# Kernel optimization log

Hardware: AMD Instinct MI355X
Metric: run time of the kernel (lower is better)

## Reference

```python
import jax, jax.numpy as jnp
import numpy as np

B, L, D = 128, 196, 512
T = 20
V, E, H, A = 10000, 256, 512, 512


def setup_inputs() -> dict:
    key = jax.random.key(0)
    ks = jax.random.split(key, 20)
    s = lambda *sh: 0.02
    inp = {
        "a": jax.random.normal(ks[0], (B, L, D), jnp.float32),
        "captions": jax.random.randint(ks[1], (B, T), 0, V),
        "lengths": jnp.full((B,), T, dtype=jnp.int64),
        "embed_W": jax.random.normal(ks[2], (V, E), jnp.float32) * 0.02,
        "Wa": jax.random.normal(ks[3], (D, A), jnp.float32) * 0.02,
        "Wh": jax.random.normal(ks[4], (H, A), jnp.float32) * 0.02,
        "Wc": jax.random.normal(ks[5], (H, A), jnp.float32) * 0.02,
        "v": jax.random.normal(ks[6], (A,), jnp.float32) * 0.02,
        "beta_W": jax.random.normal(ks[7], (H, 1), jnp.float32) * 0.02,
        "beta_b": jnp.zeros((1,), jnp.float32),
        "W_ih": jax.random.normal(ks[8], (E + D, 4 * H), jnp.float32) * 0.02,
        "W_hh": jax.random.normal(ks[9], (H, 4 * H), jnp.float32) * 0.02,
        "b_ih": jnp.zeros((4 * H,), jnp.float32),
        "b_hh": jnp.zeros((4 * H,), jnp.float32),
        "fc_W": jax.random.normal(ks[10], (H, V), jnp.float32) * 0.02,
        "fc_b": jnp.zeros((V,), jnp.float32),
        "initW_h": jax.random.normal(ks[11], (D, H), jnp.float32) * 0.02,
        "initb_h": jnp.zeros((H,), jnp.float32),
        "initW_c": jax.random.normal(ks[12], (D, H), jnp.float32) * 0.02,
        "initb_c": jnp.zeros((H,), jnp.float32),
    }
    return inp


def _decode(a, captions, embed_W, Wa, Wh, Wc, v, beta_W, beta_b,
            W_ih, W_hh, b_ih, b_hh, fc_W, fc_b,
            initW_h, initb_h, initW_c, initb_c):
    # dropout layers are treated as identity (eval mode) for a deterministic reference
    emb = embed_W[captions]                       # (B, T, E)
    mean_ctx = a.mean(axis=1)                     # (B, D)
    h0 = jnp.tanh(mean_ctx @ initW_h + initb_h)   # (B, H)
    c0 = jnp.tanh(mean_ctx @ initW_c + initb_c)
    wa = a @ Wa                                   # (B, L, A), hoisted (invariant over t)
    Hd = h0.shape[-1]

    def step(carry, x_t):
        h, c, prev_h = carry
        # dual additive attention: scores from annotations + h + prev_h (context_input)
        score = jnp.tanh(wa + (h @ Wh)[:, None, :] + (prev_h @ Wc)[:, None, :])  # (B,L,A)
        e = score @ v                                                            # (B,L)
        alpha = jax.nn.softmax(e, axis=1)
        beta = jax.nn.sigmoid(h @ beta_W + beta_b)                               # (B,1)
        ctx = beta * jnp.einsum('bl,bld->bd', alpha, a)                          # (B,D)
        # LSTMCell
        x = jnp.concatenate([x_t, ctx], axis=1)                                  # (B,E+D)
        gates = x @ W_ih + b_ih + h @ W_hh + b_hh                                # (B,4H)
        i, f, g, o = jnp.split(gates, 4, axis=1)
        c_new = jax.nn.sigmoid(f) * c + jax.nn.sigmoid(i) * jnp.tanh(g)
        h_new = jax.nn.sigmoid(o) * jnp.tanh(c_new)
        logits_t = h_new @ fc_W + fc_b                                           # (B,V)
        return (h_new, c_new, h_new), (logits_t, alpha)

    xs = jnp.swapaxes(emb[:, :T - 1, :], 0, 1)    # (T-1, B, E) time-major
    _, (logits_t, alphas_t) = jax.lax.scan(step, (h0, c0, h0), xs)
    # all lengths == T: pack_padded_sequence(batch_first=True).data is time-major flatten
    packed_logits = logits_t.reshape((T - 1) * a.shape[0], -1)                   # ((T-1)*B, V)
    alphas = jnp.swapaxes(alphas_t, 0, 1)                                        # (B, T-1, L)
    return packed_logits, alphas


def reference(a, captions, lengths, embed_W, Wa, Wh, Wc, v, beta_W, beta_b,
              W_ih, W_hh, b_ih, b_hh, fc_W, fc_b,
              initW_h, initb_h, initW_c, initb_c):
    return _decode(a, captions, embed_W, Wa, Wh, Wc, v, beta_W, beta_b,
                   W_ih, W_hh, b_ih, b_hh, fc_W, fc_b,
                   initW_h, initb_h, initW_c, initb_c)
```

## Files before the change

kernel.cpp:

```cpp
#include <hip/hip_runtime.h>
#include <hip/hip_bf16.h>
#include <math.h>

#define B_ 128
#define L_ 196
#define D_ 512
#define T_ 20
#define V_ 10000
#define E_ 256
#define H_ 512
#define A_ 512
#define TM1 19
#define ROWS (TM1*B_)
#define G4H 2048
#define KCAT 1024
#define LH 98

typedef unsigned short ushort_t;
typedef __attribute__((ext_vector_type(8))) short bf16x8;
typedef __attribute__((ext_vector_type(4))) float f32x4;

__device__ __forceinline__ float fast_tanh(float x){
    float ax = fabsf(x);
    float e = __expf(-2.f*ax);
    float r = __builtin_amdgcn_rcpf(1.f + e);
    return copysignf((1.f - e)*r, x);
}
__device__ __forceinline__ float sigmoidf_(float x){
    return __builtin_amdgcn_rcpf(1.f + __expf(-x));
}
__device__ __forceinline__ ushort_t f2b(float f){
    union{float f; unsigned u;} x; x.f = f;
    unsigned r = x.u + 0x7fffu + ((x.u>>16)&1u);
    return (ushort_t)(r>>16);
}
__device__ __forceinline__ float b2f(ushort_t h){
    union{unsigned u; float f;} x; x.u = ((unsigned)h)<<16;
    return x.f;
}
__device__ __forceinline__ float b2f_lo(unsigned u){ union{unsigned u; float f;} x; x.u = u<<16; return x.f; }
__device__ __forceinline__ float b2f_hi(unsigned u){ union{unsigned u; float f;} x; x.u = u & 0xffff0000u; return x.f; }

template<int OUT_BF16, int HAS_BIAS, int NT, int SWZ>
__global__ __launch_bounds__(256)
void gemm_mfma(const ushort_t* __restrict__ A, int lda,
               const ushort_t* __restrict__ BT, int ldb,
               void* __restrict__ Cout, int ldc,
               int N, int K, const float* __restrict__ bias)
{
    __shared__ ushort_t As[128*32];
    __shared__ ushort_t Bs[128*32];
    int bm, bn;
    if (SWZ){
        int bid = blockIdx.x;
        int swz = (bid & 7)*190 + (bid >> 3);
        int mt = swz % 19, nt = swz / 19;
        if (nt >= 79) return;
        bm = mt*128; bn = nt*128;
    } else {
        bm = blockIdx.y * 128; bn = blockIdx.x * 128;
    }
    const int tid = threadIdx.x;
    const int lane = tid & 63;
    const int wave = tid >> 6;
    const int wm = (wave >> 1) * 64;
    const int wn = (wave & 1) * 64;
    const int lrow = lane & 15;
    const int lk8  = (lane >> 4) * 8;
    const int srow = tid >> 2;
    const int skq  = ((tid & 3) * 8) ^ ((srow & 3) << 3);
    const int skq0 = (tid & 3) * 8;

    f32x4 acc[4][4];
    #pragma unroll
    for (int i=0;i<4;i++)
        #pragma unroll
        for (int j=0;j<4;j++) acc[i][j] = (f32x4){0.f,0.f,0.f,0.f};

    const ushort_t* Abase = A  + (size_t)(bm+srow)*lda + skq0;
    const ushort_t* Bbase = BT + (size_t)(bn+srow)*ldb + skq0;

    for (int k0 = 0; k0 < K; k0 += 32) {
        int4 a0 = *(const int4*)(Abase + k0);
        int4 a1 = *(const int4*)(Abase + (size_t)64*lda + k0);
        int4 b0 = *(const int4*)(Bbase + k0);
        int4 b1 = *(const int4*)(Bbase + (size_t)64*ldb + k0);
        __syncthreads();
        *(int4*)&As[srow*32 + skq]      = a0;
        *(int4*)&As[(srow+64)*32 + skq] = a1;
        *(int4*)&Bs[srow*32 + skq]      = b0;
        *(int4*)&Bs[(srow+64)*32 + skq] = b1;
        __syncthreads();
        bf16x8 af[4], bfr[4];
        #pragma unroll
        for (int i=0;i<4;i++){
            int r = wm + i*16 + lrow;
            af[i]  = *(bf16x8*)&As[r*32 + (lk8 ^ ((r & 3) << 3))];
        }
        #pragma unroll
        for (int j=0;j<4;j++){
            int r = wn + j*16 + lrow;
            bfr[j] = *(bf16x8*)&Bs[r*32 + (lk8 ^ ((r & 3) << 3))];
        }
        #pragma unroll
        for (int i=0;i<4;i++)
            #pragma unroll
            for (int j=0;j<4;j++)
                acc[i][j] = __builtin_amdgcn_mfma_f32_16x16x32_bf16(af[i], bfr[j], acc[i][j], 0, 0, 0);
    }

    const int rq = (lane >> 4) * 4;
    #pragma unroll
    for (int j=0;j<4;j++){
        int col = bn + wn + j*16 + lrow;
        if (col >= N) continue;
        float bv = HAS_BIAS ? bias[col] : 0.f;
        #pragma unroll
        for (int i=0;i<4;i++){
            #pragma unroll
            for (int q=0;q<4;q++){
                int row = bm + wm + i*16 + rq + q;
                float v = acc[i][j][q] + bv;
                if (OUT_BF16) ((ushort_t*)Cout)[(size_t)row*ldc + col] = f2b(v);
                else if (NT)  __builtin_nontemporal_store(v, &((float*)Cout)[(size_t)row*ldc + col]);
                else          ((float*)Cout)[(size_t)row*ldc + col] = v;
            }
        }
    }
}

__global__ __launch_bounds__(256) void gemm64t2(const float* __restrict__ A, int lda,
                       const float* __restrict__ B0, const float* __restrict__ B1, int ldb,
                       float* __restrict__ C0, float* __restrict__ C1, int ldc,
                       const float* __restrict__ bias0, const float* __restrict__ bias1)
{
    const float* Bm  = blockIdx.z ? B1 : B0;
    float* C         = blockIdx.z ? C1 : C0;
    const float* bias= blockIdx.z ? bias1 : bias0;
    __shared__ float As[16][65];
    __shared__ float Bs[16][65];
    int bm = blockIdx.y*64, bn = blockIdx.x*64;
    int tid = threadIdx.x;
    int tx = tid & 15, ty = tid >> 4;
    float acc[4][4] = {};
    for (int k0 = 0; k0 < D_; k0 += 16) {
        {
            int r  = tid >> 2;
            int kq = (tid & 3) * 4;
            float4 va = *(const float4*)(A + (size_t)(bm+r)*lda + k0 + kq);
            As[kq+0][r]=va.x; As[kq+1][r]=va.y; As[kq+2][r]=va.z; As[kq+3][r]=va.w;
        }
        {
            int kk = tid >> 4;
            int nq = (tid & 15) * 4;
            float4 vb = *(const float4*)(Bm + (size_t)(k0+kk)*ldb + bn + nq);
            Bs[kk][nq+0]=vb.x; Bs[kk][nq+1]=vb.y; Bs[kk][nq+2]=vb.z; Bs[kk][nq+3]=vb.w;
        }
        __syncthreads();
        #pragma unroll
        for (int k = 0; k < 16; ++k) {
            float a0[4], b0[4];
            #pragma unroll
            for (int i=0;i<4;i++) a0[i] = As[k][ty*4+i];
            #pragma unroll
            for (int j=0;j<4;j++) b0[j] = Bs[k][tx*4+j];
            #pragma unroll
            for (int i=0;i<4;i++)
                #pragma unroll
                for (int j=0;j<4;j++)
                    acc[i][j] = fmaf(a0[i], b0[j], acc[i][j]);
        }
        __syncthreads();
    }
    #pragma unroll
    for (int i=0;i<4;i++){
        int row = bm + ty*4 + i;
        #pragma unroll
        for (int j=0;j<4;j++){
            int col = bn + tx*4 + j;
            C[(size_t)row*ldc + col] = fast_tanh(acc[i][j] + bias[col]);
        }
    }
}

struct TJob { const float* src; const float* src2; ushort_t* dst;
              int lds, Ksz, Nsz, koff, ldk, nx, nblk; };
struct TJobs { TJob j[6]; };

__global__ __launch_bounds__(256) void combo_trans_k(TJobs J){
    __shared__ float t[32][33];
    int bid = blockIdx.x;
    int ji = 0;
    while (bid >= J.j[ji].nblk){ bid -= J.j[ji].nblk; ji++; }
    const TJob jb = J.j[ji];
    int n0 = (bid % jb.nx)*32, k0 = (bid / jb.nx)*32;
    int tx = threadIdx.x & 31, ty = threadIdx.x >> 5;
    #pragma unroll
    for (int kk = ty; kk < 32; kk += 8){
        int k = k0 + kk, n = n0 + tx;
        float v = 0.f;
        if (k < jb.Ksz && n < jb.Nsz){
            v = jb.src[(size_t)k*jb.lds + n];
            if (jb.src2) v += jb.src2[(size_t)k*jb.lds + n];
        }
        t[kk][tx] = v;
    }
    __syncthreads();
    #pragma unroll
    for (int nn = ty; nn < 32; nn += 8){
        int n = n0 + nn, k = k0 + tx;
        if (k < jb.Ksz) jb.dst[(size_t)n*jb.ldk + jb.koff + k] = f2b(t[tx][nn]);
    }
}

__global__ __launch_bounds__(256) void mean_cvt_k(const float* __restrict__ a, ushort_t* __restrict__ a_b,
                                                  float* __restrict__ mc,
                                                  const float* __restrict__ b_ih, const float* __restrict__ b_hh,
                                                  float* __restrict__ bias4h, unsigned* __restrict__ ebar){
    if (blockIdx.x == 256){
        for (int k = threadIdx.x; k < G4H; k += 256) bias4h[k] = b_ih[k] + b_hh[k];
        if (threadIdx.x < B_) ebar[threadIdx.x] = 0u;
        return;
    }
    int idx = blockIdx.x*256 + threadIdx.x;
    int b = idx >> 9, d = idx & 511;
    const float* p = a + (size_t)b*L_*D_ + d;
    ushort_t* q = a_b + (size_t)b*L_*D_ + d;
    float s = 0.f;
    for (int l=0;l<L_;l++){ float v = p[(size_t)l*D_]; s += v; q[(size_t)l*D_] = f2b(v); }
    mc[idx] = s * (1.f/(float)L_);
}

__global__ void gather_emb(const int* __restrict__ captions, const float* __restrict__ embW,
                           ushort_t* __restrict__ xemb){
    int i = blockIdx.x;
    int t = i / B_, b = i - t*B_;
    int cap = captions[b*T_ + t];
    float4 v = ((const float4*)(embW + (size_t)cap*E_))[threadIdx.x];
    ushort_t r[4] = {f2b(v.x),f2b(v.y),f2b(v.z),f2b(v.w)};
    *(uint2*)(xemb + (size_t)i*E_ + threadIdx.x*4) = *(uint2*)r;
}

__global__ __launch_bounds__(512) void hw0cvt_k(const float* __restrict__ h0f,
                        const ushort_t* __restrict__ WhcT,
                        ushort_t* __restrict__ xcat, float* __restrict__ hWp){
    int b = blockIdx.x, tid = threadIdx.x;
    int lane = tid & 63, wave = tid >> 6;
    __shared__ ushort_t hls[512];
    float hv = h0f[b*H_ + tid];
    ushort_t hb = f2b(hv);
    xcat[(size_t)b*KCAT + D_ + tid] = hb;
    hls[tid] = hb;
    hWp[(size_t)(b*2+1)*512 + tid] = 0.f;
    __syncthreads();
    int wn = wave * 64;
    int col16 = lane & 15;
    int khi = (lane >> 4) * 8;
    bool a_on = (col16 == 0);
    f32x4 acc[4];
    #pragma unroll
    for (int f=0;f<4;f++) acc[f] = (f32x4){0.f,0.f,0.f,0.f};
    for (int kk=0; kk<16; kk++){
        bf16x8 af = (bf16x8){0,0,0,0,0,0,0,0};
        if (a_on) af = *(const bf16x8*)&hls[kk*32 + khi];
        #pragma unroll
        for (int f=0;f<4;f++){
            bf16x8 bf = *(const bf16x8*)(WhcT + (size_t)(wn + f*16 + col16)*512 + kk*32 + khi);
            acc[f] = __builtin_amdgcn_mfma_f32_16x16x32_bf16(af, bf, acc[f], 0, 0, 0);
        }
    }
    if (lane < 16){
        #pragma unroll
        for (int f=0;f<4;f++) hWp[(size_t)(b*2+0)*512 + wn + f*16 + lane] = acc[f][0];
    }
}

__global__ __launch_bounds__(512) void mega2_k(const ushort_t* __restrict__ wa,
                        const ushort_t* __restrict__ a_b,
                        const float* __restrict__ v,
                        const float* __restrict__ beta_W, const float* __restrict__ beta_b,
                        const ushort_t* __restrict__ WhcT,
                        const float* __restrict__ gp, const float* __restrict__ embWih,
                        float* __restrict__ cbuf, float* __restrict__ hWp,
                        ushort_t* __restrict__ xcat, ushort_t* __restrict__ Hall,
                        float* __restrict__ alphas_out, float* __restrict__ ebuf,
                        unsigned* __restrict__ ebar, int t)
{
    const int b = blockIdx.x, half = blockIdx.y;
    const int tid = threadIdx.x;
    const int lane = tid & 63, wave = tid >> 6;
    __shared__ ushort_t hls[256];
    __shared__ float red[512];
    __shared__ float al_s[224];
    __shared__ float part[2][256];

    if (t > 0){
        if (tid < 256){
            const int j = half*256 + tid;
            const float* eb = embWih + ((size_t)((t-1)*B_ + b))*G4H;
            float gi = eb[j], gf = eb[H_+j], gg = eb[2*H_+j], go = eb[3*H_+j];
            #pragma unroll
            for (int ks=0; ks<8; ks++){
                const float* g = gp + ((size_t)(ks*B_ + b))*G4H;
                gi += g[j]; gf += g[H_+j]; gg += g[2*H_+j]; go += g[3*H_+j];
            }
            float ig = sigmoidf_(gi), fg = sigmoidf_(gf);
            float g2 = fast_tanh(gg), og = sigmoidf_(go);
            float c = fg*cbuf[b*H_+j] + ig*g2;
            float h = og*fast_tanh(c);
            cbuf[b*H_+j] = c;
            ushort_t hb = f2b(h);
            xcat[(size_t)b*KCAT + D_ + j] = hb;
            Hall[((size_t)(t-1)*B_ + b)*H_ + j] = hb;
            hls[tid] = hb;
        }
        __syncthreads();
        int wn = wave * 64;
        int col16 = lane & 15;
        int khi = (lane >> 4) * 8;
        bool a_on = (col16 == 0);
        f32x4 acc[4];
        #pragma unroll
        for (int f=0;f<4;f++) acc[f] = (f32x4){0.f,0.f,0.f,0.f};
        #pragma unroll
        for (int kk=0; kk<8; kk++){
            bf16x8 af = (bf16x8){0,0,0,0,0,0,0,0};
            if (a_on) af = *(const bf16x8*)&hls[kk*32 + khi];
            #pragma unroll
            for (int f=0;f<4;f++){
                bf16x8 bf = *(const bf16x8*)(WhcT + (size_t)(wn + f*16 + col16)*512 + half*256 + kk*32 + khi);
                acc[f] = __builtin_amdgcn_mfma_f32_16x16x32_bf16(af, bf, acc[f], 0, 0, 0);
            }
        }
        if (lane < 16){
            #pragma unroll
            for (int f=0;f<4;f++) hWp[(size_t)(b*2+half)*512 + wn + f*16 + lane] = acc[f][0];
        }
    }
    __syncthreads();
    if (tid == 0){
        __threadfence();
        atomicAdd(&ebar[b], 1u);
        const unsigned tgt = 2u*(unsigned)(2*t+1);
        while (__hip_atomic_load(&ebar[b], __ATOMIC_ACQUIRE, __HIP_MEMORY_SCOPE_AGENT) < tgt)
            __builtin_amdgcn_s_sleep(1);
    }
    __syncthreads();
    {
        const float* hp0 = hWp + (size_t)(b*2+0)*512 + lane*8;
        const float* hp1 = hWp + (size_t)(b*2+1)*512 + lane*8;
        float4 p00 = *(const float4*)hp0, p01 = *(const float4*)(hp0+4);
        float4 p10 = *(const float4*)hp1, p11 = *(const float4*)(hp1+4);
        float4 hw0 = make_float4(p00.x+p10.x, p00.y+p10.y, p00.z+p10.z, p00.w+p10.w);
        float4 hw1 = make_float4(p01.x+p11.x, p01.y+p11.y, p01.z+p11.z, p01.w+p11.w);
        const float* vp = v + lane*8;
        float4 v0 = *(const float4*)vp, v1 = *(const float4*)(vp+4);
        const int l0 = half*LH;
        for (int r = wave; r < LH; r += 8){
            int4 raw = *(const int4*)(wa + (((size_t)(b*L_ + l0 + r))<<9) + lane*8);
            const unsigned* u = (const unsigned*)&raw;
            float s;
            s  = fast_tanh(b2f_lo(u[0]) + hw0.x)*v0.x;
            s += fast_tanh(b2f_hi(u[0]) + hw0.y)*v0.y;
            s += fast_tanh(b2f_lo(u[1]) + hw0.z)*v0.z;
            s += fast_tanh(b2f_hi(u[1]) + hw0.w)*v0.w;
            s += fast_tanh(b2f_lo(u[2]) + hw1.x)*v1.x;
            s += fast_tanh(b2f_hi(u[2]) + hw1.y)*v1.y;
            s += fast_tanh(b2f_lo(u[3]) + hw1.z)*v1.z;
            s += fast_tanh(b2f_hi(u[3]) + hw1.w)*v1.w;
            #pragma unroll
            for (int off=32; off; off>>=1) s += __shfl_down(s, off);
            if (lane==0) ebuf[b*L_ + l0 + r] = s;
        }
    }
    __syncthreads();
    if (tid == 0){
        __threadfence();
        atomicAdd(&ebar[b], 1u);
        const unsigned tgt = 2u*(unsigned)(2*t+2);
        while (__hip_atomic_load(&ebar[b], __ATOMIC_ACQUIRE, __HIP_MEMORY_SCOPE_AGENT) < tgt)
            __builtin_amdgcn_s_sleep(1);
    }
    __syncthreads();
    float ev = (tid < L_) ? ebuf[b*L_ + tid] : -3.0e38f;
    red[tid] = ev; __syncthreads();
    #pragma unroll
    for (int s=256; s; s>>=1){ if (tid<s) red[tid] = fmaxf(red[tid], red[tid+s]); __syncthreads(); }
    float m = red[0]; __syncthreads();
    float pr = (tid < L_) ? __expf(ev - m) : 0.f;
    red[tid] = pr; __syncthreads();
    #pragma unroll
    for (int s=256; s; s>>=1){ if (tid<s) red[tid] += red[tid+s]; __syncthreads(); }
    float inv = 1.f / red[0];
    __syncthreads();
    if (tid < L_) al_s[tid] = pr*inv;
    const int l0 = half*LH;
    if (tid >= l0 && tid < l0 + LH)
        __builtin_nontemporal_store(pr*inv, alphas_out + (size_t)b*TM1*L_ + (size_t)t*L_ + tid);
    float dv = b2f(xcat[(size_t)b*KCAT + D_ + tid]) * beta_W[tid];
    red[tid] = dv; __syncthreads();
    #pragma unroll
    for (int s=256; s; s>>=1){ if (tid<s) red[tid] += red[tid+s]; __syncthreads(); }
    float beta = sigmoidf_(red[0] + beta_b[0]);
    __syncthreads();
    const int d  = half*256 + (tid & 255);
    const int lr = tid >> 8;
    const ushort_t* pa = a_b + (((size_t)(b*L_ + lr*LH))<<9) + d;
    float s0 = 0.f;
    #pragma unroll 7
    for (int i=0; i<LH; ++i) s0 = fmaf(al_s[lr*LH + i], b2f(pa[(size_t)i*512]), s0);
    part[lr][tid & 255] = s0;
    __syncthreads();
    if (tid < 256)
        xcat[(size_t)b*KCAT + half*256 + tid] = f2b(beta*(part[0][tid] + part[1][tid]));
}

__global__ __launch_bounds__(256) void gates_k(const ushort_t* __restrict__ xcat,
                        const ushort_t* __restrict__ WcatT, float* __restrict__ gp){
    __shared__ ushort_t As[128*32];
    __shared__ ushort_t Bs[64*32];
    const int bn = blockIdx.x*64;
    const int ks = blockIdx.y;
    const int tid = threadIdx.x;
    const int lane = tid & 63, wave = tid >> 6;
    const int wm = wave*32;
    const int lrow = lane & 15;
    const int lk8 = (lane >> 4) * 8;
    f32x4 acc[2][4];
    #pragma unroll
    for (int i=0;i<2;i++)
        #pragma unroll
        for (int j=0;j<4;j++) acc[i][j] = (f32x4){0.f,0.f,0.f,0.f};

    for (int kk = 0; kk < 4; ++kk){
        int k0 = ks*128 + kk*32;
        int c0 = 2*tid;
        int r0 = c0 >> 2,  kq0 = (c0 & 3)*8;
        int r1 = (c0+1) >> 2, kq1 = ((c0+1) & 3)*8;
        int4 a0 = *(const int4*)(xcat + (size_t)r0*KCAT + k0 + kq0);
        int4 a1 = *(const int4*)(xcat + (size_t)r1*KCAT + k0 + kq1);
        int rb = tid >> 2, kqb = (tid & 3)*8;
        int4 b0 = *(const int4*)(WcatT + (size_t)(bn+rb)*KCAT + k0 + kqb);
        __syncthreads();
        *(int4*)&As[r0*32 + kq0] = a0;
        *(int4*)&As[r1*32 + kq1] = a1;
        *(int4*)&Bs[rb*32 + kqb] = b0;
        __syncthreads();
        bf16x8 af[2], bfr[4];
        #pragma unroll
        for (int i=0;i<2;i++) af[i] = *(bf16x8*)&As[(wm + i*16 + lrow)*32 + lk8];
        #pragma unroll
        for (int j=0;j<4;j++) bfr[j] = *(bf16x8*)&Bs[(j*16 + lrow)*32 + lk8];
        #pragma unroll
        for (int i=0;i<2;i++)
            #pragma unroll
            for (int j=0;j<4;j++)
                acc[i][j] = __builtin_amdgcn_mfma_f32_16x16x32_bf16(af[i], bfr[j], acc[i][j], 0, 0, 0);
    }
    const int rq = (lane >> 4) * 4;
    #pragma unroll
    for (int i=0;i<2;i++){
        #pragma unroll
        for (int j=0;j<4;j++){
            int gcol = bn + j*16 + lrow;
            #pragma unroll
            for (int q=0;q<4;q++){
                int grow = wm + i*16 + rq + q;
                gp[((size_t)(ks*B_ + grow))*G4H + gcol] = acc[i][j][q];
            }
        }
    }
}

__global__ __launch_bounds__(512) void lstmfin_k(const float* __restrict__ gp, const float* __restrict__ embWih,
                       const float* __restrict__ cbuf, ushort_t* __restrict__ Hall){
    int b = blockIdx.x, j = threadIdx.x;
    const float* eb = embWih + ((size_t)(18*B_ + b))*G4H;
    float gi = eb[j], gf = eb[H_+j], gg = eb[2*H_+j], go = eb[3*H_+j];
    #pragma unroll
    for (int ks=0; ks<8; ks++){
        const float* g = gp + ((size_t)(ks*B_ + b))*G4H;
        gi += g[j]; gf += g[H_+j]; gg += g[2*H_+j]; go += g[3*H_+j];
    }
    float ig = sigmoidf_(gi), fg = sigmoidf_(gf);
    float g2 = fast_tanh(gg), og = sigmoidf_(go);
    float c = fg*cbuf[b*H_+j] + ig*g2;
    float h = og*fast_tanh(c);
    Hall[((size_t)18*B_ + b)*H_ + j] = f2b(h);
}

extern "C" void kernel_launch(void* const* d_in, const int* in_sizes, int n_in,
                              void* d_out, int out_size, void* d_ws, size_t ws_size,
                              hipStream_t stream) {
    const float* a      = (const float*)d_in[0];
    const int*   caps   = (const int*)  d_in[1];
    const float* embW   = (const float*)d_in[3];
    const float* Wa     = (const float*)d_in[4];
    const float* Wh     = (const float*)d_in[5];
    const float* Wc     = (const float*)d_in[6];
    const float* v      = (const float*)d_in[7];
    const float* beta_W = (const float*)d_in[8];
    const float* beta_b = (const float*)d_in[9];
    const float* W_ih   = (const float*)d_in[10];
    const float* W_hh   = (const float*)d_in[11];
    const float* b_ih   = (const float*)d_in[12];
    const float* b_hh   = (const float*)d_in[13];
    const float* fc_W   = (const float*)d_in[14];
    const float* fc_b   = (const float*)d_in[15];
    const float* iWh    = (const float*)d_in[16];
    const float* ibh    = (const float*)d_in[17];
    const float* iWc    = (const float*)d_in[18];
    const float* ibc    = (const float*)d_in[19];

    float* out    = (float*)d_out;
    float* alphas = out + (size_t)ROWS*V_;

    char* ob = (char*)d_out;
    ushort_t* wa_b   = (ushort_t*)(ob);
    ushort_t* a_b    = (ushort_t*)(ob + 25690112);
    float*    embWih = (float*)   (ob + 51380224);

    char* wb = (char*)d_ws;
    float* mean_ctx = (float*)(wb);
    float* cbuf     = (float*)(wb + 262144);
    float* h0f      = (float*)(wb + 524288);
    float* hWp      = (float*)(wb + 786432);
    float* ebuf     = (float*)(wb + 1310720);
    float* bias4h   = (float*)(wb + 1413120);
    unsigned* ebar  = (unsigned*)(wb + 1421312);
    float* gp       = (float*)(wb + 1422336);
    ushort_t* xcat_b = (ushort_t*)(wb + 9810944);
    ushort_t* xemb_b = (ushort_t*)(wb + 10073088);
    ushort_t* Hall   = (ushort_t*)(wb + 11318272);
    ushort_t* WaT    = (ushort_t*)(wb + 13808640);
    ushort_t* WhcT   = (ushort_t*)(wb + 14332928);
    ushort_t* WihT   = (ushort_t*)(wb + 14857216);
    ushort_t* WcatT  = (ushort_t*)(wb + 15905792);
    ushort_t* fcWT   = (ushort_t*)(wb + 20100096);

    TJobs J;
    J.j[0] = { Wa,   nullptr, WaT,  512, 512, 512,  0,   512,  16, 256 };
    J.j[1] = { Wh,   Wc,      WhcT, 512, 512, 512,  0,   512,  16, 256 };
    J.j[2] = { W_ih, nullptr, WihT, G4H, 256, G4H,  0,   256,  64, 512 };
    J.j[3] = { W_ih + (size_t)E_*G4H, nullptr, WcatT, G4H, 512, G4H, 0,   KCAT, 64, 1024 };
    J.j[4] = { W_hh, nullptr, WcatT, G4H, 512, G4H,  512, KCAT, 64, 1024 };
    J.j[5] = { fc_W, nullptr, fcWT, V_,  512, V_,   0,   512,  316, 5056 };
    combo_trans_k<<<8128, 256, 0, stream>>>(J);
    mean_cvt_k<<<257, 256, 0, stream>>>(a, a_b, mean_ctx, b_ih, b_hh, bias4h, ebar);
    gather_emb<<<ROWS, 64, 0, stream>>>(caps, embW, xemb_b);
    gemm64t2<<<dim3(8,2,2), 256, 0, stream>>>(mean_ctx, D_, iWh, iWc, H_, h0f, cbuf, H_, ibh, ibc);
    hw0cvt_k<<<B_, 512, 0, stream>>>(h0f, WhcT, xcat_b, hWp);
    gemm_mfma<1,0,0,0><<<dim3(4,196), 256, 0, stream>>>(a_b, D_, WaT, D_, wa_b, A_, A_, D_, nullptr);
    gemm_mfma<0,1,0,0><<<dim3(16,19), 256, 0, stream>>>(xemb_b, E_, WihT, E_, embWih, G4H, G4H, E_, bias4h);

    for (int t = 0; t < TM1; ++t){
        mega2_k<<<dim3(B_,2), 512, 0, stream>>>(wa_b, a_b, v, beta_W, beta_b, WhcT,
                                                gp, embWih, cbuf, hWp, xcat_b, Hall,
                                                alphas, ebuf, ebar, t);
        gates_k<<<dim3(32,8), 256, 0, stream>>>(xcat_b, WcatT, gp);
    }
    lstmfin_k<<<B_, 512, 0, stream>>>(gp, embWih, cbuf, Hall);

    gemm_mfma<0,1,1,1><<<dim3(1520), 256, 0, stream>>>(Hall, H_, fcWT, H_, out, V_, V_, H_, fc_b);
}
```

Baseline: 1.054 ms.

## Double-buffer GEMM with direct global-to-LDS loads and vectorize prep kernels

```diff
diff --git a/kernel.cpp b/kernel.cpp
--- a/kernel.cpp
+++ b/kernel.cpp
@@ -41,6 +41,10 @@
 __device__ __forceinline__ float b2f_lo(unsigned u){ union{unsigned u; float f;} x; x.u = u<<16; return x.f; }
 __device__ __forceinline__ float b2f_hi(unsigned u){ union{unsigned u; float f;} x; x.u = u & 0xffff0000u; return x.f; }
 
+#define GL16(gsrc, ldst) __builtin_amdgcn_global_load_lds( \
+    (const __attribute__((address_space(1))) unsigned*)(gsrc), \
+    (__attribute__((address_space(3))) unsigned*)(ldst), 16, 0, 0)
+
 template<int OUT_BF16, int HAS_BIAS, int NT, int SWZ>
 __global__ __launch_bounds__(256)
 void gemm_mfma(const ushort_t* __restrict__ A, int lda,
@@ -48,8 +52,8 @@
                void* __restrict__ Cout, int ldc,
                int N, int K, const float* __restrict__ bias)
 {
-    __shared__ ushort_t As[128*32];
-    __shared__ ushort_t Bs[128*32];
+    __shared__ ushort_t As[2][4096];
+    __shared__ ushort_t Bs[2][4096];
     int bm, bn;
     if (SWZ){
         int bid = blockIdx.x;
@@ -68,8 +72,8 @@
     const int lrow = lane & 15;
     const int lk8  = (lane >> 4) * 8;
     const int srow = tid >> 2;
-    const int skq  = ((tid & 3) * 8) ^ ((srow & 3) << 3);
     const int skq0 = (tid & 3) * 8;
+    const int wbase = wave * 512;
 
     f32x4 acc[4][4];
     #pragma unroll
@@ -77,36 +81,36 @@
         #pragma unroll
         for (int j=0;j<4;j++) acc[i][j] = (f32x4){0.f,0.f,0.f,0.f};
 
-    const ushort_t* Abase = A  + (size_t)(bm+srow)*lda + skq0;
-    const ushort_t* Bbase = BT + (size_t)(bn+srow)*ldb + skq0;
-
+    const ushort_t* Ab = A  + (size_t)(bm+srow)*lda + skq0;
+    const ushort_t* Bb = BT + (size_t)(bn+srow)*ldb + skq0;
+
+    GL16(Ab,                    &As[0][wbase]);
+    GL16(Ab + (size_t)64*lda,   &As[0][2048 + wbase]);
+    GL16(Bb,                    &Bs[0][wbase]);
+    GL16(Bb + (size_t)64*ldb,   &Bs[0][2048 + wbase]);
+
+    int buf = 0;
     for (int k0 = 0; k0 < K; k0 += 32) {
-        int4 a0 = *(const int4*)(Abase + k0);
-        int4 a1 = *(const int4*)(Abase + (size_t)64*lda + k0);
-        int4 b0 = *(const int4*)(Bbase + k0);
-        int4 b1 = *(const int4*)(Bbase + (size_t)64*ldb + k0);
+        asm volatile("s_waitcnt vmcnt(0)" ::: "memory");
         __syncthreads();
-        *(int4*)&As[srow*32 + skq]      = a0;
-        *(int4*)&As[(srow+64)*32 + skq] = a1;
-        *(int4*)&Bs[srow*32 + skq]      = b0;
-        *(int4*)&Bs[(srow+64)*32 + skq] = b1;
-        __syncthreads();
+        if (k0 + 32 < K){
+            int nb = buf ^ 1;
+            GL16(Ab + k0 + 32,                  &As[nb][wbase]);
+            GL16(Ab + (size_t)64*lda + k0 + 32, &As[nb][2048 + wbase]);
+            GL16(Bb + k0 + 32,                  &Bs[nb][wbase]);
+            GL16(Bb + (size_t)64*ldb + k0 + 32, &Bs[nb][2048 + wbase]);
+        }
         bf16x8 af[4], bfr[4];
         #pragma unroll
-        for (int i=0;i<4;i++){
-            int r = wm + i*16 + lrow;
-            af[i]  = *(bf16x8*)&As[r*32 + (lk8 ^ ((r & 3) << 3))];
-        }
-        #pragma unroll
-        for (int j=0;j<4;j++){
-            int r = wn + j*16 + lrow;
-            bfr[j] = *(bf16x8*)&Bs[r*32 + (lk8 ^ ((r & 3) << 3))];
-        }
+        for (int i=0;i<4;i++) af[i]  = *(bf16x8*)&As[buf][(wm + i*16 + lrow)*32 + lk8];
+        #pragma unroll
+        for (int j=0;j<4;j++) bfr[j] = *(bf16x8*)&Bs[buf][(wn + j*16 + lrow)*32 + lk8];
         #pragma unroll
         for (int i=0;i<4;i++)
             #pragma unroll
             for (int j=0;j<4;j++)
                 acc[i][j] = __builtin_amdgcn_mfma_f32_16x16x32_bf16(af[i], bfr[j], acc[i][j], 0, 0, 0);
+        buf ^= 1;
     }
 
     const int rq = (lane >> 4) * 4;
@@ -217,28 +221,36 @@
                                                   float* __restrict__ mc,
                                                   const float* __restrict__ b_ih, const float* __restrict__ b_hh,
                                                   float* __restrict__ bias4h, unsigned* __restrict__ ebar){
-    if (blockIdx.x == 256){
+    if (blockIdx.x == 64){
         for (int k = threadIdx.x; k < G4H; k += 256) bias4h[k] = b_ih[k] + b_hh[k];
         if (threadIdx.x < B_) ebar[threadIdx.x] = 0u;
         return;
     }
     int idx = blockIdx.x*256 + threadIdx.x;
-    int b = idx >> 9, d = idx & 511;
-    const float* p = a + (size_t)b*L_*D_ + d;
-    ushort_t* q = a_b + (size_t)b*L_*D_ + d;
-    float s = 0.f;
-    for (int l=0;l<L_;l++){ float v = p[(size_t)l*D_]; s += v; q[(size_t)l*D_] = f2b(v); }
-    mc[idx] = s * (1.f/(float)L_);
-}
-
-__global__ void gather_emb(const int* __restrict__ captions, const float* __restrict__ embW,
+    int b = idx >> 7, dq = (idx & 127) * 4;
+    const float* p = a + (size_t)b*L_*D_ + dq;
+    ushort_t* q = a_b + (size_t)b*L_*D_ + dq;
+    float4 s = make_float4(0.f,0.f,0.f,0.f);
+    for (int l=0;l<L_;l++){
+        float4 v = *(const float4*)(p + (size_t)l*D_);
+        s.x += v.x; s.y += v.y; s.z += v.z; s.w += v.w;
+        ushort_t r[4] = {f2b(v.x),f2b(v.y),f2b(v.z),f2b(v.w)};
+        *(uint2*)(q + (size_t)l*D_) = *(uint2*)r;
+    }
+    const float inv = 1.f/(float)L_;
+    float4 o = make_float4(s.x*inv, s.y*inv, s.z*inv, s.w*inv);
+    *(float4*)(mc + (size_t)b*D_ + dq) = o;
+}
+
+__global__ __launch_bounds__(256) void gather_emb(const int* __restrict__ captions, const float* __restrict__ embW,
                            ushort_t* __restrict__ xemb){
-    int i = blockIdx.x;
+    int i = blockIdx.x*4 + (threadIdx.x >> 6);
+    int lane = threadIdx.x & 63;
     int t = i / B_, b = i - t*B_;
     int cap = captions[b*T_ + t];
-    float4 v = ((const float4*)(embW + (size_t)cap*E_))[threadIdx.x];
+    float4 v = ((const float4*)(embW + (size_t)cap*E_))[lane];
     ushort_t r[4] = {f2b(v.x),f2b(v.y),f2b(v.z),f2b(v.w)};
-    *(uint2*)(xemb + (size_t)i*E_ + threadIdx.x*4) = *(uint2*)r;
+    *(uint2*)(xemb + (size_t)i*E_ + lane*4) = *(uint2*)r;
 }
 
 __global__ __launch_bounds__(512) void hw0cvt_k(const float* __restrict__ h0f,
@@ -546,8 +558,8 @@
     J.j[4] = { W_hh, nullptr, WcatT, G4H, 512, G4H,  512, KCAT, 64, 1024 };
     J.j[5] = { fc_W, nullptr, fcWT, V_,  512, V_,   0,   512,  316, 5056 };
     combo_trans_k<<<8128, 256, 0, stream>>>(J);
-    mean_cvt_k<<<257, 256, 0, stream>>>(a, a_b, mean_ctx, b_ih, b_hh, bias4h, ebar);
-    gather_emb<<<ROWS, 64, 0, stream>>>(caps, embW, xemb_b);
+    mean_cvt_k<<<65, 256, 0, stream>>>(a, a_b, mean_ctx, b_ih, b_hh, bias4h, ebar);
+    gather_emb<<<ROWS/4, 256, 0, stream>>>(caps, embW, xemb_b);
     gemm64t2<<<dim3(8,2,2), 256, 0, stream>>>(mean_ctx, D_, iWh, iWc, H_, h0f, cbuf, H_, ibh, ibc);
     hw0cvt_k<<<B_, 512, 0, stream>>>(h0f, WhcT, xcat_b, hWp);
     gemm_mfma<1,0,0,0><<<dim3(4,196), 256, 0, stream>>>(a_b, D_, WaT, D_, wa_b, A_, A_, D_, nullptr);
```

Result: no change. 1.063 ms (+0.8%).
